# Optimization experiments

Measured on AMD Instinct MI355X. Metric: run time of the kernel, lower is better.

Reference implementation:

```python
import jax, jax.numpy as jnp
import numpy as np

WIDTH = 2048
NUM_HEADS = 16
HEAD_DIM = WIDTH // NUM_HEADS
BATCH = 16384


def block_diag_linear(x, w, b):
    # x: [..., width] -> [..., h, i] einsum with w: [h, i, j]
    xh = x.reshape(x.shape[:-1] + (NUM_HEADS, HEAD_DIM))
    y = jnp.einsum('...hi,hij->...hj', xh, w) + b
    return y.reshape(x.shape)


def setup_inputs() -> dict:
    key = jax.random.key(0)
    ks = jax.random.split(key, 7)
    x = jax.random.normal(ks[0], (BATCH, WIDTH), dtype=jnp.float32)
    state = jax.random.normal(ks[1], (BATCH, WIDTH), dtype=jnp.float32)
    w_in = jax.random.normal(ks[2], (NUM_HEADS, HEAD_DIM, HEAD_DIM), dtype=jnp.float32) * 0.02
    b_in = jax.random.normal(ks[3], (NUM_HEADS, HEAD_DIM), dtype=jnp.float32) * 0.02
    w_a = jax.random.normal(ks[4], (NUM_HEADS, HEAD_DIM, HEAD_DIM), dtype=jnp.float32) * 0.02
    b_a = jax.random.normal(ks[5], (NUM_HEADS, HEAD_DIM), dtype=jnp.float32) * 0.02
    a_param = jax.random.normal(ks[6], (WIDTH,), dtype=jnp.float32) * 0.5
    return {'x': x, 'state': state, 'w_in': w_in, 'b_in': b_in,
            'w_a': w_a, 'b_a': b_a, 'a_param': a_param}


def reference(x, state, w_in, b_in, w_a, b_a, a_param):
    gate_x = jax.nn.sigmoid(block_diag_linear(x, w_in, b_in))
    gate_a = jax.nn.sigmoid(block_diag_linear(x, w_a, b_a))
    log_a = -8.0 * gate_a * jax.nn.softplus(a_param)  # [B, width]
    a = jnp.exp(log_a)
    scale = jnp.sqrt(1.0 - jnp.exp(2.0 * log_a))
    return a * state + gate_x * x * scale
```

## Files before the change

kernel.cpp:

```cpp
#include <hip/hip_runtime.h>

typedef __attribute__((ext_vector_type(8))) short bf16x8;
typedef __attribute__((ext_vector_type(4))) float f32x4;
typedef __attribute__((ext_vector_type(4))) unsigned short u16x4;

#define WIDTH  2048
#define NHEADS 16
#define HDIM   128
#define BM     64

__device__ __forceinline__ unsigned short f2bf(float f) {
  union { float f; unsigned int u; } v; v.f = f;
  unsigned int u = v.u;
  unsigned int r = (u + 0x7FFFu + ((u >> 16) & 1u)) >> 16;
  return (unsigned short)r;
}

__device__ __forceinline__ float bf2f(unsigned short s) {
  union { unsigned int u; float f; } v;
  v.u = ((unsigned int)s) << 16;
  return v.f;
}

__global__ __launch_bounds__(256) void prep_kernel(
    const float* __restrict__ w_in, const float* __restrict__ w_a,
    const float* __restrict__ a_param,
    unsigned short* __restrict__ wTin, unsigned short* __restrict__ wTa,
    float* __restrict__ sp8) {
  int tid = blockIdx.x * 256 + threadIdx.x;
  int h   = tid >> 14;
  int rem = tid & 16383;
  int j   = rem >> 7;
  int i   = rem & 127;
  int src = (h << 14) + (i << 7) + j;
  wTin[tid] = f2bf(w_in[src]);
  wTa[tid]  = f2bf(w_a[src]);
  if (tid < WIDTH) {
    float v  = a_param[tid];
    float sp = (v > 20.0f) ? v : log1pf(__expf(v));
    sp8[tid] = 8.0f * sp;
  }
}

__global__ __launch_bounds__(256, 3) void rglru_kernel(
    const float* __restrict__ x, const float* __restrict__ state,
    const float* __restrict__ b_in, const float* __restrict__ b_a,
    const unsigned short* __restrict__ wTin, const unsigned short* __restrict__ wTa,
    const float* __restrict__ sp8, float* __restrict__ out) {
  __shared__ unsigned short xs[BM * HDIM];

  const int bid  = blockIdx.x;
  const int h    = bid & (NHEADS - 1);
  const int rb   = bid >> 4;
  const int t    = threadIdx.x;
  const int lane = t & 63;
  const int wid  = t >> 6;
  const int l15  = lane & 15;
  const int l4   = lane >> 4;

  const float* xtile = x + (long)rb * BM * WIDTH + h * HDIM;
#pragma unroll
  for (int it = 0; it < 8; ++it) {
    int idx = it * 256 + t;
    int r   = idx >> 5;
    int c4  = idx & 31;
    f32x4 v = __builtin_nontemporal_load(
        reinterpret_cast<const f32x4*>(xtile + (long)r * WIDTH) + c4);
    uint2 p;
    p.x = (unsigned int)f2bf(v.x) | ((unsigned int)f2bf(v.y) << 16);
    p.y = (unsigned int)f2bf(v.z) | ((unsigned int)f2bf(v.w) << 16);
    int off = (r * 256 + c4 * 8) ^ ((r & 7) << 4);
    *reinterpret_cast<uint2*>(reinterpret_cast<char*>(xs) + off) = p;
  }
  __syncthreads();

  f32x4 sreg[2][4];
  f32x4 bi4[2], ba4[2], sp4[2];
#pragma unroll
  for (int n = 0; n < 2; ++n) {
    int colh0 = wid * 32 + n * 16 + l4 * 4;
    int col0  = h * HDIM + colh0;
#pragma unroll
    for (int m = 0; m < 4; ++m) {
      long row = (long)(rb * BM + m * 16 + l15);
      sreg[n][m] = __builtin_nontemporal_load(
          reinterpret_cast<const f32x4*>(state + row * WIDTH + col0));
    }
    bi4[n] = *reinterpret_cast<const f32x4*>(b_in + h * HDIM + colh0);
    ba4[n] = *reinterpret_cast<const f32x4*>(b_a + h * HDIM + colh0);
    sp4[n] = *reinterpret_cast<const f32x4*>(sp8 + col0);
  }

  f32x4 acc_in[4][2], acc_a[4][2];
#pragma unroll
  for (int m = 0; m < 4; ++m)
#pragma unroll
    for (int n = 0; n < 2; ++n) {
      acc_in[m][n] = (f32x4)(0.0f);
      acc_a[m][n]  = (f32x4)(0.0f);
    }

  const unsigned short* wbin = wTin + ((h * HDIM + wid * 32) * HDIM);
  const unsigned short* wba  = wTa  + ((h * HDIM + wid * 32) * HDIM);

#pragma unroll
  for (int kk = 0; kk < 4; ++kk) {
    bf16x8 xfr[4];
#pragma unroll
    for (int m = 0; m < 4; ++m) {
      int row  = m * 16 + l15;
      int boff = (row * 256 + kk * 64 + l4 * 16) ^ ((row & 7) << 4);
      xfr[m] = *reinterpret_cast<const bf16x8*>(
          reinterpret_cast<const char*>(xs) + boff);
    }
    bf16x8 win[2], wa[2];
#pragma unroll
    for (int n = 0; n < 2; ++n) {
      int widx = (n * 16 + l15) * HDIM + kk * 32 + l4 * 8;
      win[n] = *reinterpret_cast<const bf16x8*>(wbin + widx);
      wa[n]  = *reinterpret_cast<const bf16x8*>(wba + widx);
    }
#pragma unroll
    for (int m = 0; m < 4; ++m)
#pragma unroll
      for (int n = 0; n < 2; ++n) {
        acc_in[m][n] = __builtin_amdgcn_mfma_f32_16x16x32_bf16(
            win[n], xfr[m], acc_in[m][n], 0, 0, 0);
        acc_a[m][n] = __builtin_amdgcn_mfma_f32_16x16x32_bf16(
            wa[n], xfr[m], acc_a[m][n], 0, 0, 0);
      }
  }

#pragma unroll
  for (int n = 0; n < 2; ++n) {
    int colh0 = wid * 32 + n * 16 + l4 * 4;
    int col0  = h * HDIM + colh0;
    f32x4 bi = bi4[n], bav = ba4[n], sp = sp4[n];
#pragma unroll
    for (int m = 0; m < 4; ++m) {
      int lrow = m * 16 + l15;
      long off = (long)(rb * BM + lrow) * WIDTH + col0;
      int xoff = (lrow * 256 + colh0 * 2) ^ ((lrow & 7) << 4);
      u16x4 xb = *reinterpret_cast<const u16x4*>(
          reinterpret_cast<const char*>(xs) + xoff);
      f32x4 sv = sreg[n][m];
      f32x4 o;
#pragma unroll
      for (int r = 0; r < 4; ++r) {
        float yin = acc_in[m][n][r] + bi[r];
        float ya  = acc_a[m][n][r] + bav[r];
        float gx = __builtin_amdgcn_rcpf(1.0f + __expf(-yin));
        float ga = __builtin_amdgcn_rcpf(1.0f + __expf(-ya));
        float av = __expf(-ga * sp[r]);
        float sc = sqrtf(fmaxf(1.0f - av * av, 0.0f));
        o[r] = av * sv[r] + gx * bf2f(xb[r]) * sc;
      }
      __builtin_nontemporal_store(o, reinterpret_cast<f32x4*>(out + off));
    }
  }
}

extern "C" void kernel_launch(void* const* d_in, const int* in_sizes, int n_in,
                              void* d_out, int out_size, void* d_ws, size_t ws_size,
                              hipStream_t stream) {
  const float* x       = (const float*)d_in[0];
  const float* state   = (const float*)d_in[1];
  const float* w_in    = (const float*)d_in[2];
  const float* b_in    = (const float*)d_in[3];
  const float* w_a     = (const float*)d_in[4];
  const float* b_a     = (const float*)d_in[5];
  const float* a_param = (const float*)d_in[6];
  float* out = (float*)d_out;

  unsigned short* wTin = (unsigned short*)d_ws;
  unsigned short* wTa  = wTin + NHEADS * HDIM * HDIM;
  float*          sp8  = (float*)(wTa + NHEADS * HDIM * HDIM);

  hipLaunchKernelGGL(prep_kernel, dim3(1024), dim3(256), 0, stream,
                     w_in, w_a, a_param, wTin, wTa, sp8);

  hipLaunchKernelGGL(rglru_kernel, dim3(4096), dim3(256), 0, stream,
                     x, state, b_in, b_a, wTin, wTa, sp8, out);
}
```

Baseline: 119.5 us.

## Make blocks loop over row tiles with double-buffered x prefetch

Each block now processes eight 64-row tiles for one head instead of one. While the current tile computes, the next tile's x is loaded into registers and then staged into a second LDS buffer. This overlaps global loads with MFMA and epilogue work and amortizes the bias and weight setup. In exchange it launches far fewer blocks, lowers the occupancy hint, drops the nontemporal load and store hints, and loads state only after the matmul, which may expose latency.

```diff
diff --git a/kernel.cpp b/kernel.cpp
--- a/kernel.cpp
+++ b/kernel.cpp
@@ -8,6 +8,7 @@
 #define NHEADS 16
 #define HDIM   128
 #define BM     64
+#define TPB    8
 
 __device__ __forceinline__ unsigned short f2bf(float f) {
   union { float f; unsigned int u; } v; v.f = f;
@@ -42,120 +43,145 @@
   }
 }
 
-__global__ __launch_bounds__(256, 3) void rglru_kernel(
+__global__ __launch_bounds__(256, 2) void rglru_kernel(
     const float* __restrict__ x, const float* __restrict__ state,
     const float* __restrict__ b_in, const float* __restrict__ b_a,
     const unsigned short* __restrict__ wTin, const unsigned short* __restrict__ wTa,
     const float* __restrict__ sp8, float* __restrict__ out) {
-  __shared__ unsigned short xs[BM * HDIM];
+  __shared__ unsigned short xs[2][BM * HDIM];
 
   const int bid  = blockIdx.x;
   const int h    = bid & (NHEADS - 1);
-  const int rb   = bid >> 4;
+  const int rg0  = (bid >> 4) * TPB;
   const int t    = threadIdx.x;
   const int lane = t & 63;
   const int wid  = t >> 6;
   const int l15  = lane & 15;
   const int l4   = lane >> 4;
 
-  const float* xtile = x + (long)rb * BM * WIDTH + h * HDIM;
-#pragma unroll
-  for (int it = 0; it < 8; ++it) {
-    int idx = it * 256 + t;
-    int r   = idx >> 5;
-    int c4  = idx & 31;
-    f32x4 v = __builtin_nontemporal_load(
-        reinterpret_cast<const f32x4*>(xtile + (long)r * WIDTH) + c4);
-    uint2 p;
-    p.x = (unsigned int)f2bf(v.x) | ((unsigned int)f2bf(v.y) << 16);
-    p.y = (unsigned int)f2bf(v.z) | ((unsigned int)f2bf(v.w) << 16);
-    int off = (r * 256 + c4 * 8) ^ ((r & 7) << 4);
-    *reinterpret_cast<uint2*>(reinterpret_cast<char*>(xs) + off) = p;
-  }
-  __syncthreads();
-
-  f32x4 sreg[2][4];
+  const int r_  = t >> 5;
+  const int c4_ = t & 31;
+
+  const float* xbase = x + h * HDIM;
+  f32x4 xa[8];
+
+  auto issue = [&](int tt) {
+    long row0 = (long)(rg0 + tt) * BM;
+#pragma unroll
+    for (int it = 0; it < 8; ++it) {
+      int r = it * 8 + r_;
+      xa[it] = *reinterpret_cast<const f32x4*>(
+          xbase + (row0 + r) * WIDTH + c4_ * 4);
+    }
+  };
+  auto commit = [&](int buf) {
+#pragma unroll
+    for (int it = 0; it < 8; ++it) {
+      int r = it * 8 + r_;
+      uint2 p;
+      p.x = (unsigned int)f2bf(xa[it][0]) | ((unsigned int)f2bf(xa[it][1]) << 16);
+      p.y = (unsigned int)f2bf(xa[it][2]) | ((unsigned int)f2bf(xa[it][3]) << 16);
+      int off = (r * 256 + c4_ * 8) ^ ((r & 7) << 4);
+      *reinterpret_cast<uint2*>(reinterpret_cast<char*>(xs[buf]) + off) = p;
+    }
+  };
+
+  const unsigned short* wbin = wTin + ((h * HDIM + wid * 32) * HDIM);
+  const unsigned short* wba  = wTa  + ((h * HDIM + wid * 32) * HDIM);
   f32x4 bi4[2], ba4[2], sp4[2];
 #pragma unroll
   for (int n = 0; n < 2; ++n) {
     int colh0 = wid * 32 + n * 16 + l4 * 4;
-    int col0  = h * HDIM + colh0;
-#pragma unroll
-    for (int m = 0; m < 4; ++m) {
-      long row = (long)(rb * BM + m * 16 + l15);
-      sreg[n][m] = __builtin_nontemporal_load(
-          reinterpret_cast<const f32x4*>(state + row * WIDTH + col0));
-    }
     bi4[n] = *reinterpret_cast<const f32x4*>(b_in + h * HDIM + colh0);
     ba4[n] = *reinterpret_cast<const f32x4*>(b_a + h * HDIM + colh0);
-    sp4[n] = *reinterpret_cast<const f32x4*>(sp8 + col0);
+    sp4[n] = *reinterpret_cast<const f32x4*>(sp8 + h * HDIM + colh0);
   }
 
-  f32x4 acc_in[4][2], acc_a[4][2];
-#pragma unroll
-  for (int m = 0; m < 4; ++m)
+  issue(0);
+
+  for (int tt = 0; tt < TPB; ++tt) {
+    const int buf = tt & 1;
+    commit(buf);
+    asm volatile("s_waitcnt lgkmcnt(0)" ::: "memory");
+    __builtin_amdgcn_s_barrier();
+    __builtin_amdgcn_sched_barrier(0);
+
+    if (tt + 1 < TPB) issue(tt + 1);
+
+    const long row0 = (long)(rg0 + tt) * BM;
+
+    f32x4 acc_in[4][2], acc_a[4][2];
+#pragma unroll
+    for (int m = 0; m < 4; ++m)
+#pragma unroll
+      for (int n = 0; n < 2; ++n) {
+        acc_in[m][n] = (f32x4)(0.0f);
+        acc_a[m][n]  = (f32x4)(0.0f);
+      }
+
+#pragma unroll
+    for (int kk = 0; kk < 4; ++kk) {
+      bf16x8 xfr[4];
+#pragma unroll
+      for (int m = 0; m < 4; ++m) {
+        int row  = m * 16 + l15;
+        int boff = (row * 256 + kk * 64 + l4 * 16) ^ ((row & 7) << 4);
+        xfr[m] = *reinterpret_cast<const bf16x8*>(
+            reinterpret_cast<const char*>(xs[buf]) + boff);
+      }
+      bf16x8 win[2], wa[2];
+#pragma unroll
+      for (int n = 0; n < 2; ++n) {
+        int widx = (n * 16 + l15) * HDIM + kk * 32 + l4 * 8;
+        win[n] = *reinterpret_cast<const bf16x8*>(wbin + widx);
+        wa[n]  = *reinterpret_cast<const bf16x8*>(wba + widx);
+      }
+#pragma unroll
+      for (int m = 0; m < 4; ++m)
+#pragma unroll
+        for (int n = 0; n < 2; ++n) {
+          acc_in[m][n] = __builtin_amdgcn_mfma_f32_16x16x32_bf16(
+              win[n], xfr[m], acc_in[m][n], 0, 0, 0);
+          acc_a[m][n] = __builtin_amdgcn_mfma_f32_16x16x32_bf16(
+              wa[n], xfr[m], acc_a[m][n], 0, 0, 0);
+        }
+    }
+
+    f32x4 sv[2][4];
 #pragma unroll
     for (int n = 0; n < 2; ++n) {
-      acc_in[m][n] = (f32x4)(0.0f);
-      acc_a[m][n]  = (f32x4)(0.0f);
-    }
-
-  const unsigned short* wbin = wTin + ((h * HDIM + wid * 32) * HDIM);
-  const unsigned short* wba  = wTa  + ((h * HDIM + wid * 32) * HDIM);
-
-#pragma unroll
-  for (int kk = 0; kk < 4; ++kk) {
-    bf16x8 xfr[4];
-#pragma unroll
-    for (int m = 0; m < 4; ++m) {
-      int row  = m * 16 + l15;
-      int boff = (row * 256 + kk * 64 + l4 * 16) ^ ((row & 7) << 4);
-      xfr[m] = *reinterpret_cast<const bf16x8*>(
-          reinterpret_cast<const char*>(xs) + boff);
-    }
-    bf16x8 win[2], wa[2];
+      int colh0 = wid * 32 + n * 16 + l4 * 4;
+#pragma unroll
+      for (int m = 0; m < 4; ++m) {
+        long off = (row0 + m * 16 + l15) * WIDTH + h * HDIM + colh0;
+        sv[n][m] = *reinterpret_cast<const f32x4*>(state + off);
+      }
+    }
+
 #pragma unroll
     for (int n = 0; n < 2; ++n) {
-      int widx = (n * 16 + l15) * HDIM + kk * 32 + l4 * 8;
-      win[n] = *reinterpret_cast<const bf16x8*>(wbin + widx);
-      wa[n]  = *reinterpret_cast<const bf16x8*>(wba + widx);
-    }
-#pragma unroll
-    for (int m = 0; m < 4; ++m)
-#pragma unroll
-      for (int n = 0; n < 2; ++n) {
-        acc_in[m][n] = __builtin_amdgcn_mfma_f32_16x16x32_bf16(
-            win[n], xfr[m], acc_in[m][n], 0, 0, 0);
-        acc_a[m][n] = __builtin_amdgcn_mfma_f32_16x16x32_bf16(
-            wa[n], xfr[m], acc_a[m][n], 0, 0, 0);
-      }
-  }
-
-#pragma unroll
-  for (int n = 0; n < 2; ++n) {
-    int colh0 = wid * 32 + n * 16 + l4 * 4;
-    int col0  = h * HDIM + colh0;
-    f32x4 bi = bi4[n], bav = ba4[n], sp = sp4[n];
-#pragma unroll
-    for (int m = 0; m < 4; ++m) {
-      int lrow = m * 16 + l15;
-      long off = (long)(rb * BM + lrow) * WIDTH + col0;
-      int xoff = (lrow * 256 + colh0 * 2) ^ ((lrow & 7) << 4);
-      u16x4 xb = *reinterpret_cast<const u16x4*>(
-          reinterpret_cast<const char*>(xs) + xoff);
-      f32x4 sv = sreg[n][m];
-      f32x4 o;
-#pragma unroll
-      for (int r = 0; r < 4; ++r) {
-        float yin = acc_in[m][n][r] + bi[r];
-        float ya  = acc_a[m][n][r] + bav[r];
-        float gx = __builtin_amdgcn_rcpf(1.0f + __expf(-yin));
-        float ga = __builtin_amdgcn_rcpf(1.0f + __expf(-ya));
-        float av = __expf(-ga * sp[r]);
-        float sc = sqrtf(fmaxf(1.0f - av * av, 0.0f));
-        o[r] = av * sv[r] + gx * bf2f(xb[r]) * sc;
-      }
-      __builtin_nontemporal_store(o, reinterpret_cast<f32x4*>(out + off));
+      int colh0 = wid * 32 + n * 16 + l4 * 4;
+      f32x4 bi = bi4[n], bav = ba4[n], sp = sp4[n];
+#pragma unroll
+      for (int m = 0; m < 4; ++m) {
+        int lrow = m * 16 + l15;
+        long off = (row0 + lrow) * WIDTH + h * HDIM + colh0;
+        int xoff = (lrow * 256 + colh0 * 2) ^ ((lrow & 7) << 4);
+        u16x4 xb = *reinterpret_cast<const u16x4*>(
+            reinterpret_cast<const char*>(xs[buf]) + xoff);
+        f32x4 o;
+#pragma unroll
+        for (int r = 0; r < 4; ++r) {
+          float yin = acc_in[m][n][r] + bi[r];
+          float ya  = acc_a[m][n][r] + bav[r];
+          float gx = __builtin_amdgcn_rcpf(1.0f + __expf(-yin));
+          float ga = __builtin_amdgcn_rcpf(1.0f + __expf(-ya));
+          float av = __expf(-ga * sp[r]);
+          float sc = sqrtf(fmaxf(1.0f - av * av, 0.0f));
+          o[r] = av * sv[n][m][r] + gx * bf2f(xb[r]) * sc;
+        }
+        *reinterpret_cast<f32x4*>(out + off) = o;
+      }
     }
   }
 }
@@ -179,6 +205,6 @@
   hipLaunchKernelGGL(prep_kernel, dim3(1024), dim3(256), 0, stream,
                      w_in, w_a, a_param, wTin, wTa, sp8);
 
-  hipLaunchKernelGGL(rglru_kernel, dim3(4096), dim3(256), 0, stream,
+  hipLaunchKernelGGL(rglru_kernel, dim3(4096 / TPB), dim3(256), 0, stream,
                      x, state, b_in, b_a, wTin, wTa, sp8, out);
 }
```

Measured after the change: 117.4 us. About the same (-1.7%).
